# Performance work log

Measured on AMD Instinct MI355X. Metric: run time of the kernel, lower is better.

Reference implementation:

```python
import jax, jax.numpy as jnp
import numpy as np
from jax import lax


def ternarize(w):
    # w: (O, I, KH, KW). Per-output-filter delta/alpha as in the torch code.
    O = w.shape[0]
    n = w[0].size  # elements per filter
    abs_w = jnp.abs(w)
    flat_abs = abs_w.reshape(O, -1)
    delta = (0.7 / n) * flat_abs.sum(axis=1)          # (O,)
    d = delta.reshape(O, 1, 1, 1)
    mask = abs_w > d                                   # |w| > delta
    cnt = mask.reshape(O, -1).sum(axis=1).astype(w.dtype)  # (O,)
    alpha = jnp.where(mask, abs_w, 0.0).reshape(O, -1).sum(axis=1) / cnt  # (O,)
    tern = jnp.where(w > d, 1.0, jnp.where(w < -d, -1.0, 0.0)).astype(w.dtype)
    return tern * alpha.reshape(O, 1, 1, 1)


def conv2d(x, w, stride=(1, 1), padding=((1, 1), (1, 1))):
    return lax.conv_general_dilated(
        x, w, window_strides=stride, padding=padding,
        dimension_numbers=("NCHW", "OIHW", "NCHW"))


def setup_inputs() -> dict:
    key = jax.random.key(0)
    k1, k2, k3 = jax.random.split(key, 3)
    x = jax.random.normal(k1, (32, 256, 56, 56), dtype=jnp.float32)
    # kaiming-uniform-ish, clamped to [-1, 1] as in __init__
    weight = jnp.clip(jax.random.normal(k2, (256, 256, 3, 3), dtype=jnp.float32) * 0.05, -1.0, 1.0)
    bias = jax.random.normal(k3, (256,), dtype=jnp.float32) * 0.02
    return {"x": x, "weight": weight, "bias": bias}


def reference(x, weight, bias):
    w_t = ternarize(weight)
    y = conv2d(x, w_t) + bias[None, :, None, None]
    return y
```

## Files before the change

### kernel.cpp

```cpp
#include <hip/hip_runtime.h>
#include <hip/hip_bf16.h>
#include <stdint.h>

typedef short bf16x8 __attribute__((ext_vector_type(8)));
typedef float f32x4 __attribute__((ext_vector_type(4)));
typedef unsigned short ushort_t;
typedef unsigned int uint_t;

#define CIN   256
#define COUT  256
#define HWDIM 56
#define IMG   (HWDIM * HWDIM)
#define K_TOT (CIN * 9)
#define NIMG  32
#define NPIX  (NIMG * IMG)
#define BM    128
#define BN    128
#define NCHUNK 36

#define AS1CAST(p) ((const __attribute__((address_space(1))) unsigned int*)(uintptr_t)(p))
#define AS3CAST(p) ((__attribute__((address_space(3))) unsigned int*)(uintptr_t)(p))

__device__ __forceinline__ ushort_t f2bf(float f) {
    union { float f; uint_t u; } v; v.f = f;
    uint_t u = v.u;
    uint_t r = u + 0x7FFFu + ((u >> 16) & 1u);
    return (ushort_t)(r >> 16);
}

__global__ __launch_bounds__(256) void ternarize_kernel(
        const float* __restrict__ w,
        ushort_t* __restrict__ wt2,
        float* __restrict__ alpha_out,
        ushort_t* __restrict__ xt_pad_row) {
    const int o = blockIdx.x;
    const int t = threadIdx.x;
    const int lane = t & 63;
    const int wv = t >> 6;
    const float* base = w + (size_t)o * K_TOT;

    if (o == 0 && t < 32) ((uint4*)xt_pad_row)[t] = (uint4){0u, 0u, 0u, 0u};

    float v[9];
#pragma unroll
    for (int i = 0; i < 9; ++i) v[i] = base[t + 256 * i];

    __shared__ float sred[8];

    float s = 0.f;
#pragma unroll
    for (int i = 0; i < 9; ++i) s += fabsf(v[i]);
#pragma unroll
    for (int off = 32; off > 0; off >>= 1) s += __shfl_down(s, off);
    if (lane == 0) sred[wv] = s;
    __syncthreads();
    if (t == 0) sred[0] = sred[0] + sred[1] + sred[2] + sred[3];
    __syncthreads();
    const float delta = (0.7f / (float)K_TOT) * sred[0];
    __syncthreads();

    float asum = 0.f, cnt = 0.f;
#pragma unroll
    for (int i = 0; i < 9; ++i) {
        float a = fabsf(v[i]);
        if (a > delta) { asum += a; cnt += 1.f; }
    }
#pragma unroll
    for (int off = 32; off > 0; off >>= 1) {
        asum += __shfl_down(asum, off);
        cnt  += __shfl_down(cnt, off);
    }
    if (lane == 0) { sred[wv] = asum; sred[4 + wv] = cnt; }
    __syncthreads();
    if (t == 0) {
        float at = sred[0] + sred[1] + sred[2] + sred[3];
        float ct = sred[4] + sred[5] + sred[6] + sred[7];
        alpha_out[o] = at / ct;
    }

#pragma unroll
    for (int i = 0; i < 9; ++i) {
        int idx = t + 256 * i;
        int c = idx / 9;
        int r = idx - c * 9;
        float x = v[i];
        ushort_t bits = 0;
        if (x > delta)       bits = 0x3F80u;
        else if (x < -delta) bits = 0xBF80u;
        wt2[(size_t)o * K_TOT + r * 256 + c] = bits;
    }
}

__global__ __launch_bounds__(256) void transpose_kernel(
        const float* __restrict__ x, ushort_t* __restrict__ xt) {
    __shared__ float L[32][132];
    const int hw0 = blockIdx.x * 32;
    const int c0  = blockIdx.y * 128;
    const int n   = blockIdx.z;
    const int t = threadIdx.x;
    const int c_ = t >> 1;
    const int half = t & 1;

    const float* src = x + (size_t)(n * CIN + c0 + c_) * IMG + hw0 + half * 16;
    float4 v[4];
#pragma unroll
    for (int k = 0; k < 4; ++k) v[k] = *(const float4*)(src + k * 4);
#pragma unroll
    for (int k = 0; k < 4; ++k) {
        L[half * 16 + k * 4 + 0][c_] = v[k].x;
        L[half * 16 + k * 4 + 1][c_] = v[k].y;
        L[half * 16 + k * 4 + 2][c_] = v[k].z;
        L[half * 16 + k * 4 + 3][c_] = v[k].w;
    }
    __syncthreads();

    const int seg = t & 15;
    const int hwb = t >> 4;
#pragma unroll
    for (int j = 0; j < 2; ++j) {
        const int hwl = hwb + j * 16;
        const float2* row = (const float2*)&L[hwl][seg * 8];
        uint_t pk[4];
#pragma unroll
        for (int q = 0; q < 4; ++q) {
            float2 f = row[q];
            pk[q] = (uint_t)f2bf(f.x) | ((uint_t)f2bf(f.y) << 16);
        }
        *(uint4*)&xt[(size_t)(n * IMG + hw0 + hwl) * CIN + c0 + seg * 8] =
            (uint4){pk[0], pk[1], pk[2], pk[3]};
    }
}

__global__ __launch_bounds__(256, 2) void tern_conv_kernel(
        const ushort_t* __restrict__ xt,
        const ushort_t* __restrict__ wt2,
        const float* __restrict__ alpha,
        const float* __restrict__ bias,
        float* __restrict__ out) {
    __shared__ __align__(16) ushort_t As[2][BM * 64];
    __shared__ __align__(16) ushort_t Xs[2][BN * 64];

    const int tid = threadIdx.x;
    const int wv = tid >> 6;
    const int l = tid & 63;
    const int bid = blockIdx.x;
    const int o0 = (bid & 1) * BM;
    const int p0 = (bid >> 1) * BN;

    const int rthr = tid >> 3;
    const int g = (l & 7) ^ ((l >> 3) & 7);

    const ushort_t* abase[4];
    int ximg[4], xh[4], xw[4];
#pragma unroll
    for (int i = 0; i < 4; ++i) {
        abase[i] = wt2 + (size_t)(o0 + i * 32 + rthr) * K_TOT + g * 8;
        int p = p0 + i * 32 + rthr;
        int n_img = p / IMG;
        int hw_ = p - n_img * IMG;
        xh[i] = hw_ / HWDIM;
        xw[i] = hw_ - xh[i] * HWDIM;
        ximg[i] = n_img * IMG;
    }

    int doff[4];
#pragma unroll
    for (int i = 0; i < 4; ++i) doff[i] = (i * 32 + (wv << 3)) << 6;

    const int qd = l >> 4, ln = l & 15;
    const int wm = (wv >> 1) * 64, wn = (wv & 1) * 64;
    const int so0 = (qd ^ (ln & 7)) * 8;
    int arow[4], xrow[4];
#pragma unroll
    for (int i = 0; i < 4; ++i) {
        arow[i] = (wm + i * 16 + ln) * 64;
        xrow[i] = (wn + i * 16 + ln) * 64;
    }

    f32x4 acc[4][4];
#pragma unroll
    for (int i = 0; i < 4; ++i)
#pragma unroll
        for (int j = 0; j < 4; ++j)
            acc[i][j] = (f32x4){0.f, 0.f, 0.f, 0.f};

    bf16x8 fa[2][8], fx[2][8];

#define STAGE_CHUNK(c, SLOT) do {                                               \
    const int st_ = (c) >> 1, hs_ = (c) & 1;                                    \
    const int c0_ = (st_ >= 9) ? 128 : 0;                                       \
    const int kp_ = st_ - ((st_ >= 9) ? 9 : 0);                                 \
    const int dh_ = kp_ / 3 - 1;                                                \
    const int dw_ = kp_ - (dh_ + 1) * 3 - 1;                                    \
    const int aoff_ = kp_ * 256 + c0_ + hs_ * 64;                               \
    _Pragma("unroll")                                                           \
    for (int i = 0; i < 4; ++i)                                                 \
        __builtin_amdgcn_global_load_lds(AS1CAST(abase[i] + aoff_),             \
                                         AS3CAST(&As[SLOT][doff[i]]), 16, 0, 0);\
    _Pragma("unroll")                                                           \
    for (int i = 0; i < 4; ++i) {                                               \
        int h2_ = xh[i] + dh_, w2_ = xw[i] + dw_;                               \
        int row_ = ((unsigned)h2_ < (unsigned)HWDIM &&                          \
                    (unsigned)w2_ < (unsigned)HWDIM)                            \
                       ? (ximg[i] + h2_ * HWDIM + w2_) : NPIX;                  \
        __builtin_amdgcn_global_load_lds(                                       \
            AS1CAST(xt + (size_t)row_ * CIN + c0_ + hs_ * 64 + g * 8),          \
            AS3CAST(&Xs[SLOT][doff[i]]), 16, 0, 0);                             \
    }                                                                           \
} while (0)

#define READ_FRAGS(P) do {                                                      \
    _Pragma("unroll")                                                           \
    for (int m = 0; m < 4; ++m) {                                               \
        fa[P][m]     = *(const bf16x8*)&As[P][arow[m] + so0];                   \
        fa[P][m + 4] = *(const bf16x8*)&As[P][arow[m] + (so0 ^ 32)];            \
    }                                                                           \
    _Pragma("unroll")                                                           \
    for (int n = 0; n < 4; ++n) {                                               \
        fx[P][n]     = *(const bf16x8*)&Xs[P][xrow[n] + so0];                   \
        fx[P][n + 4] = *(const bf16x8*)&Xs[P][xrow[n] + (so0 ^ 32)];            \
    }                                                                           \
} while (0)

#define MFMA_CLUSTER(P) do {                                                    \
    __builtin_amdgcn_s_setprio(1);                                              \
    _Pragma("unroll")                                                           \
    for (int m = 0; m < 4; ++m)                                                 \
        _Pragma("unroll")                                                       \
        for (int n = 0; n < 4; ++n)                                             \
            acc[m][n] = __builtin_amdgcn_mfma_f32_16x16x32_bf16(                \
                fa[P][m], fx[P][n], acc[m][n], 0, 0, 0);                        \
    _Pragma("unroll")                                                           \
    for (int m = 0; m < 4; ++m)                                                 \
        _Pragma("unroll")                                                       \
        for (int n = 0; n < 4; ++n)                                             \
            acc[m][n] = __builtin_amdgcn_mfma_f32_16x16x32_bf16(                \
                fa[P][m + 4], fx[P][n + 4], acc[m][n], 0, 0, 0);                \
    __builtin_amdgcn_s_setprio(0);                                              \
} while (0)

#define PHASE(k, P) do {                                                        \
    asm volatile("s_waitcnt vmcnt(8)" ::: "memory");                            \
    __builtin_amdgcn_s_barrier();                                               \
    asm volatile("" ::: "memory");                                              \
    READ_FRAGS(P);                                                              \
    MFMA_CLUSTER(1 - (P));                                                      \
    asm volatile("s_waitcnt lgkmcnt(0)" ::: "memory");                          \
    __builtin_amdgcn_s_barrier();                                               \
    asm volatile("" ::: "memory");                                              \
    STAGE_CHUNK((k) + 2, P);                                                    \
} while (0)

#define PHASE_TAIL(P, VM) do {                                                  \
    asm volatile("s_waitcnt vmcnt(" #VM ")" ::: "memory");                      \
    __builtin_amdgcn_s_barrier();                                               \
    asm volatile("" ::: "memory");                                              \
    READ_FRAGS(P);                                                              \
    MFMA_CLUSTER(1 - (P));                                                      \
} while (0)

    STAGE_CHUNK(0, 0);
    STAGE_CHUNK(1, 1);
    asm volatile("s_waitcnt vmcnt(8)" ::: "memory");
    __builtin_amdgcn_s_barrier();
    asm volatile("" ::: "memory");
    READ_FRAGS(0);
    asm volatile("s_waitcnt lgkmcnt(0)" ::: "memory");
    __builtin_amdgcn_s_barrier();
    asm volatile("" ::: "memory");
    STAGE_CHUNK(2, 0);

#pragma unroll 1
    for (int k = 1; k < 33; k += 2) {
        PHASE(k, 1);
        PHASE(k + 1, 0);
    }
    PHASE(33, 1);
    PHASE_TAIL(0, 8);
    PHASE_TAIL(1, 0);
    MFMA_CLUSTER(1);

#undef PHASE_TAIL
#undef PHASE
#undef MFMA_CLUSTER
#undef READ_FRAGS
#undef STAGE_CHUNK

#pragma unroll
    for (int im = 0; im < 4; ++im) {
        const int orow = o0 + wm + im * 16 + qd * 4;
        const f32x4 al = *(const f32x4*)&alpha[orow];
        const f32x4 bi = *(const f32x4*)&bias[orow];
#pragma unroll
        for (int in2 = 0; in2 < 4; ++in2) {
            const int pc = p0 + wn + in2 * 16 + ln;
            const int ni = pc / IMG;
            const int hwc = pc - ni * IMG;
            const size_t obase = (size_t)ni * COUT * IMG + hwc;
#pragma unroll
            for (int rr = 0; rr < 4; ++rr)
                out[obase + (size_t)(orow + rr) * IMG] = al[rr] * acc[im][in2][rr] + bi[rr];
        }
    }
}

extern "C" void kernel_launch(void* const* d_in, const int* in_sizes, int n_in,
                              void* d_out, int out_size, void* d_ws, size_t ws_size,
                              hipStream_t stream) {
    const float* x      = (const float*)d_in[0];
    const float* weight = (const float*)d_in[1];
    const float* bias   = (const float*)d_in[2];
    float* out = (float*)d_out;

    ushort_t* xt     = (ushort_t*)d_ws;
    ushort_t* wt2    = (ushort_t*)((char*)d_ws + (size_t)(NPIX + 1) * CIN * sizeof(ushort_t));
    float*    alphav = (float*)((char*)wt2 + (size_t)COUT * K_TOT * sizeof(ushort_t));

    ternarize_kernel<<<COUT, 256, 0, stream>>>(weight, wt2, alphav,
                                               xt + (size_t)NPIX * CIN);

    dim3 tg(IMG / 32, CIN / 128, NIMG);
    transpose_kernel<<<tg, 256, 0, stream>>>(x, xt);

    const int n_blocks = (COUT / BM) * (NPIX / BN);
    tern_conv_kernel<<<n_blocks, 256, 0, stream>>>(xt, wt2, alphav, bias, out);
}
```

Before: 306.4 us.

## Enlarge conv GEMM tile to 256x256 with 512-thread blocks and split-K MFMA schedule

Each block now covers all 256 output channels and 256 pixels, using 8 waves with 8x4 MFMA tiles per wave, so each input pixel tile is loaded only once instead of twice. The pipeline is restructured so each chunk issues the first K-half MFMAs, then stages the next chunk, then runs the second K-half. Fragment registers are no longer double-buffered. This raises LDS use (128 KB shared across two buffers) and register pressure (128 accumulator registers), which may reduce occupancy or cause spills. Block count halves, which may hurt load balance across CUs.

```diff
diff --git a/kernel.cpp b/kernel.cpp
--- a/kernel.cpp
+++ b/kernel.cpp
@@ -14,8 +14,8 @@
 #define K_TOT (CIN * 9)
 #define NIMG  32
 #define NPIX  (NIMG * IMG)
-#define BM    128
-#define BN    128
+#define BM    256
+#define BN    256
 #define NCHUNK 36
 
 #define AS1CAST(p) ((const __attribute__((address_space(1))) unsigned int*)(uintptr_t)(p))
@@ -131,7 +131,7 @@
     }
 }
 
-__global__ __launch_bounds__(256, 2) void tern_conv_kernel(
+__global__ __launch_bounds__(512, 2) void tern_conv_kernel(
         const ushort_t* __restrict__ xt,
         const ushort_t* __restrict__ wt2,
         const float* __restrict__ alpha,
@@ -143,9 +143,7 @@
     const int tid = threadIdx.x;
     const int wv = tid >> 6;
     const int l = tid & 63;
-    const int bid = blockIdx.x;
-    const int o0 = (bid & 1) * BM;
-    const int p0 = (bid >> 1) * BN;
+    const int p0 = blockIdx.x * BN;
 
     const int rthr = tid >> 3;
     const int g = (l & 7) ^ ((l >> 3) & 7);
@@ -154,8 +152,8 @@
     int ximg[4], xh[4], xw[4];
 #pragma unroll
     for (int i = 0; i < 4; ++i) {
-        abase[i] = wt2 + (size_t)(o0 + i * 32 + rthr) * K_TOT + g * 8;
-        int p = p0 + i * 32 + rthr;
+        abase[i] = wt2 + (size_t)(i * 64 + rthr) * K_TOT + g * 8;
+        int p = p0 + i * 64 + rthr;
         int n_img = p / IMG;
         int hw_ = p - n_img * IMG;
         xh[i] = hw_ / HWDIM;
@@ -165,26 +163,26 @@
 
     int doff[4];
 #pragma unroll
-    for (int i = 0; i < 4; ++i) doff[i] = (i * 32 + (wv << 3)) << 6;
+    for (int i = 0; i < 4; ++i) doff[i] = (i * 64 + wv * 8) * 64;
 
     const int qd = l >> 4, ln = l & 15;
-    const int wm = (wv >> 1) * 64, wn = (wv & 1) * 64;
+    const int wm = (wv >> 2) * 128;
+    const int wn = (wv & 3) * 64;
     const int so0 = (qd ^ (ln & 7)) * 8;
-    int arow[4], xrow[4];
-#pragma unroll
-    for (int i = 0; i < 4; ++i) {
-        arow[i] = (wm + i * 16 + ln) * 64;
-        xrow[i] = (wn + i * 16 + ln) * 64;
-    }
-
-    f32x4 acc[4][4];
-#pragma unroll
-    for (int i = 0; i < 4; ++i)
+    int arow[8], xrow[4];
+#pragma unroll
+    for (int i = 0; i < 8; ++i) arow[i] = (wm + i * 16 + ln) * 64;
+#pragma unroll
+    for (int j = 0; j < 4; ++j) xrow[j] = (wn + j * 16 + ln) * 64;
+
+    f32x4 acc[8][4];
+#pragma unroll
+    for (int i = 0; i < 8; ++i)
 #pragma unroll
         for (int j = 0; j < 4; ++j)
             acc[i][j] = (f32x4){0.f, 0.f, 0.f, 0.f};
 
-    bf16x8 fa[2][8], fx[2][8];
+    bf16x8 fa0[8], fa1[8], fx0[4], fx1[4];
 
 #define STAGE_CHUNK(c, SLOT) do {                                               \
     const int st_ = (c) >> 1, hs_ = (c) & 1;                                    \
@@ -211,84 +209,84 @@
 
 #define READ_FRAGS(P) do {                                                      \
     _Pragma("unroll")                                                           \
-    for (int m = 0; m < 4; ++m) {                                               \
-        fa[P][m]     = *(const bf16x8*)&As[P][arow[m] + so0];                   \
-        fa[P][m + 4] = *(const bf16x8*)&As[P][arow[m] + (so0 ^ 32)];            \
+    for (int m = 0; m < 8; ++m) {                                               \
+        fa0[m] = *(const bf16x8*)&As[P][arow[m] + so0];                         \
+        fa1[m] = *(const bf16x8*)&As[P][arow[m] + (so0 ^ 32)];                  \
     }                                                                           \
     _Pragma("unroll")                                                           \
     for (int n = 0; n < 4; ++n) {                                               \
-        fx[P][n]     = *(const bf16x8*)&Xs[P][xrow[n] + so0];                   \
-        fx[P][n + 4] = *(const bf16x8*)&Xs[P][xrow[n] + (so0 ^ 32)];            \
+        fx0[n] = *(const bf16x8*)&Xs[P][xrow[n] + so0];                         \
+        fx1[n] = *(const bf16x8*)&Xs[P][xrow[n] + (so0 ^ 32)];                  \
     }                                                                           \
 } while (0)
 
-#define MFMA_CLUSTER(P) do {                                                    \
+#define MFMA_K0 do {                                                            \
     __builtin_amdgcn_s_setprio(1);                                              \
     _Pragma("unroll")                                                           \
-    for (int m = 0; m < 4; ++m)                                                 \
+    for (int m = 0; m < 8; ++m)                                                 \
         _Pragma("unroll")                                                       \
         for (int n = 0; n < 4; ++n)                                             \
             acc[m][n] = __builtin_amdgcn_mfma_f32_16x16x32_bf16(                \
-                fa[P][m], fx[P][n], acc[m][n], 0, 0, 0);                        \
-    _Pragma("unroll")                                                           \
-    for (int m = 0; m < 4; ++m)                                                 \
+                fa0[m], fx0[n], acc[m][n], 0, 0, 0);                            \
+    __builtin_amdgcn_s_setprio(0);                                              \
+} while (0)
+
+#define MFMA_K1 do {                                                            \
+    __builtin_amdgcn_s_setprio(1);                                              \
+    _Pragma("unroll")                                                           \
+    for (int m = 0; m < 8; ++m)                                                 \
         _Pragma("unroll")                                                       \
         for (int n = 0; n < 4; ++n)                                             \
             acc[m][n] = __builtin_amdgcn_mfma_f32_16x16x32_bf16(                \
-                fa[P][m + 4], fx[P][n + 4], acc[m][n], 0, 0, 0);                \
+                fa1[m], fx1[n], acc[m][n], 0, 0, 0);                            \
     __builtin_amdgcn_s_setprio(0);                                              \
 } while (0)
 
-#define PHASE(k, P) do {                                                        \
+#define CHUNK_FULL(k, P) do {                                                   \
     asm volatile("s_waitcnt vmcnt(8)" ::: "memory");                            \
     __builtin_amdgcn_s_barrier();                                               \
     asm volatile("" ::: "memory");                                              \
     READ_FRAGS(P);                                                              \
-    MFMA_CLUSTER(1 - (P));                                                      \
+    MFMA_K0;                                                                    \
     asm volatile("s_waitcnt lgkmcnt(0)" ::: "memory");                          \
     __builtin_amdgcn_s_barrier();                                               \
     asm volatile("" ::: "memory");                                              \
     STAGE_CHUNK((k) + 2, P);                                                    \
-} while (0)
-
-#define PHASE_TAIL(P, VM) do {                                                  \
+    MFMA_K1;                                                                    \
+} while (0)
+
+#define CHUNK_TAIL(P, VM) do {                                                  \
     asm volatile("s_waitcnt vmcnt(" #VM ")" ::: "memory");                      \
     __builtin_amdgcn_s_barrier();                                               \
     asm volatile("" ::: "memory");                                              \
     READ_FRAGS(P);                                                              \
-    MFMA_CLUSTER(1 - (P));                                                      \
+    MFMA_K0;                                                                    \
+    MFMA_K1;                                                                    \
 } while (0)
 
     STAGE_CHUNK(0, 0);
     STAGE_CHUNK(1, 1);
-    asm volatile("s_waitcnt vmcnt(8)" ::: "memory");
-    __builtin_amdgcn_s_barrier();
-    asm volatile("" ::: "memory");
-    READ_FRAGS(0);
-    asm volatile("s_waitcnt lgkmcnt(0)" ::: "memory");
-    __builtin_amdgcn_s_barrier();
-    asm volatile("" ::: "memory");
-    STAGE_CHUNK(2, 0);
-
+
+    CHUNK_FULL(0, 0);
 #pragma unroll 1
     for (int k = 1; k < 33; k += 2) {
-        PHASE(k, 1);
-        PHASE(k + 1, 0);
-    }
-    PHASE(33, 1);
-    PHASE_TAIL(0, 8);
-    PHASE_TAIL(1, 0);
-    MFMA_CLUSTER(1);
-
-#undef PHASE_TAIL
-#undef PHASE
-#undef MFMA_CLUSTER
+        CHUNK_FULL(k, 1);
+        CHUNK_FULL(k + 1, 0);
+    }
+    CHUNK_FULL(33, 1);
+    CHUNK_TAIL(0, 8);
+    CHUNK_TAIL(1, 0);
+
+#undef CHUNK_TAIL
+#undef CHUNK_FULL
+#undef MFMA_K1
+#undef MFMA_K0
 #undef READ_FRAGS
 #undef STAGE_CHUNK
 
 #pragma unroll
-    for (int im = 0; im < 4; ++im) {
-        const int orow = o0 + wm + im * 16 + qd * 4;
+    for (int im = 0; im < 8; ++im) {
+        const int orow = wm + im * 16 + qd * 4;
         const f32x4 al = *(const f32x4*)&alpha[orow];
         const f32x4 bi = *(const f32x4*)&bias[orow];
 #pragma unroll
@@ -322,6 +320,6 @@
     dim3 tg(IMG / 32, CIN / 128, NIMG);
     transpose_kernel<<<tg, 256, 0, stream>>>(x, xt);
 
-    const int n_blocks = (COUT / BM) * (NPIX / BN);
-    tern_conv_kernel<<<n_blocks, 256, 0, stream>>>(xt, wt2, alphav, bias, out);
-}
+    const int n_blocks = NPIX / BN;
+    tern_conv_kernel<<<n_blocks, 512, 0, stream>>>(xt, wt2, alphav, bias, out);
+}
```

Result: slower. 536.3 us (+75.0%).
